# Kernel optimization log

Measured on AMD Instinct MI355X. Metric: run time of the kernel, lower is better.

The kernel has to match this reference:

```python
import jax, jax.numpy as jnp
import numpy as np

N, DIM, E = 50000, 128, 600000


def setup_inputs() -> dict:
    key = jax.random.key(0)
    ks = jax.random.split(key, 10)
    scale = 1.0 / np.sqrt(DIM)
    return {
        "s": jax.random.normal(ks[0], (N, DIM), jnp.float32),
        "v": jax.random.normal(ks[1], (N, 3, DIM), jnp.float32),
        "edge_index": jax.random.randint(ks[2], (2, E), 0, N, jnp.int32),
        # linear_q: Linear(dim, dim); stored as [in, out] so y = x @ W + b
        "Wq": jax.random.normal(ks[3], (DIM, DIM), jnp.float32) * scale,
        "bq": jnp.zeros((DIM,), jnp.float32),
        # linear_kv: Linear(dim, 3*dim)
        "Wkv": jax.random.normal(ks[4], (DIM, 3 * DIM), jnp.float32) * scale,
        "bkv": jnp.zeros((3 * DIM,), jnp.float32),
        # vec_mlp: Linear(dim, dim)
        "Wvec": jax.random.normal(ks[5], (DIM, DIM), jnp.float32) * scale,
        "bvec": jnp.zeros((DIM,), jnp.float32),
    }


def reference(s, v, edge_index, Wq, bq, Wkv, bkv, Wvec, bvec):
    n_nodes = s.shape[0]
    row, col = edge_index[0], edge_index[1]

    q = s @ Wq + bq                                   # [N, dim]
    kv = s @ Wkv + bkv                                # [N, 3*dim]
    k, v_s, v_v = jnp.split(kv, 3, axis=-1)           # each [N, dim]

    # edge attention weight: per-edge dot product of gathered q/k
    w = jnp.sum(q[row] * k[col], axis=-1, keepdims=True)   # [E, 1]

    edge_msg_s = w * v_s[col]                               # [E, dim]
    # [E,1,1] * [E,1,dim] * [E,3,dim] -> [E,3,dim]
    edge_msg_v = w[:, :, None] * v_v[col][:, None, :] * v[col]

    agg_s = jax.ops.segment_sum(edge_msg_s, row, num_segments=n_nodes)  # [N, dim]
    agg_v = jax.ops.segment_sum(edge_msg_v, row, num_segments=n_nodes)  # [N, 3, dim]

    s_out = s + agg_s
    v_out = v + (agg_v @ Wvec + bvec)
    return (s_out, v_out)
```

## Files before the change

### kernel.cpp

```cpp
#include <hip/hip_runtime.h>
#include <hip/hip_bf16.h>

typedef __attribute__((ext_vector_type(8))) __bf16 bf16x8;
typedef __attribute__((ext_vector_type(4))) float f32x4;


__global__ void prep_kernel(const int* __restrict__ row, int* __restrict__ cnt, int e,
                            const float* __restrict__ Wq, const float* __restrict__ Wkv,
                            const float* __restrict__ Wvec, const float* __restrict__ bq,
                            const float* __restrict__ bkv,
                            __bf16* __restrict__ Wt, float* __restrict__ bM,
                            float* __restrict__ m2, float* __restrict__ c0, int nbh) {
  const int bid = blockIdx.x, tid = threadIdx.x;
  if (bid < nbh) {
    int i = bid * 256 + tid;
    if (i < e) atomicAdd(&cnt[row[i]], 1);
  } else if (bid < nbh + 256) {
    int idx = (bid - nbh) * 256 + tid;
    int c = 128 + (idx >> 7), k = idx & 127;
    float w = (c < 512) ? Wkv[k * 384 + (c - 128)] : Wvec[k * 128 + (c - 512)];
    Wt[c * 128 + k] = (__bf16)w;
  } else if (bid < nbh + 256 + 128) {
    __shared__ float wk[128];
    int c = bid - (nbh + 256);
    if (tid < 128) wk[tid] = Wkv[c * 384 + tid];
    __syncthreads();
    if (tid < 128) {
      float acc = 0.f;
      #pragma unroll 8
      for (int j = 0; j < 128; j++) acc += Wq[tid * 128 + j] * wk[j];
      Wt[c * 128 + tid] = (__bf16)acc;
    } else if (tid == 128) {
      float acc = 0.f;
      for (int j = 0; j < 128; j++) acc += bq[j] * wk[j];
      bM[c] = acc;
    }
  } else {
    if (tid < 128) {
      float acc = 0.f;
      for (int j = 0; j < 128; j++) acc += Wq[tid * 128 + j] * bkv[j];
      m2[tid] = acc;
    } else if (tid == 128) {
      float acc = 0.f;
      for (int j = 0; j < 128; j++) acc += bq[j] * bkv[j];
      c0[0] = acc;
    }
  }
}

__global__ __launch_bounds__(1024) void scan1_kernel(const int* __restrict__ cnt, int* __restrict__ off,
                                                     int* __restrict__ bsum, int n) {
  __shared__ int sh[1024];
  int tid = threadIdx.x;
  int i = blockIdx.x * 1024 + tid;
  int v = (i < n) ? cnt[i] : 0;
  sh[tid] = v;
  __syncthreads();
  for (int d = 1; d < 1024; d <<= 1) {
    int t = (tid >= d) ? sh[tid - d] : 0;
    __syncthreads();
    sh[tid] += t;
    __syncthreads();
  }
  if (i < n) off[i] = sh[tid] - v;
  if (tid == 1023) bsum[blockIdx.x] = sh[1023];
}

__global__ __launch_bounds__(1024) void scan3_kernel(const int* __restrict__ bsum, int* __restrict__ off,
                                                     int* __restrict__ cursor, int n, int e) {
  __shared__ int base_sh;
  const int tid = threadIdx.x;
  if (tid < 64) {
    int part = 0;
    for (int b = tid; b < (int)blockIdx.x; b += 64) part += bsum[b];
    #pragma unroll
    for (int m = 32; m >= 1; m >>= 1) part += __shfl_xor(part, m);
    if (tid == 0) base_sh = part;
  }
  __syncthreads();
  const int base = base_sh;
  int i = blockIdx.x * 1024 + tid;
  if (i < n) { int o = off[i] + base; off[i] = o; cursor[i] = o; }
  if (i == 0) off[n] = e;
}


__global__ __launch_bounds__(256) void scatter_gemm1(
    const int* __restrict__ row, const int* __restrict__ col,
    int* __restrict__ cursor, int* __restrict__ scol, int e, int ngemm,
    const float* __restrict__ s, const __bf16* __restrict__ Wtg,
    const float* __restrict__ bM, const float* __restrict__ bkv,
    const float* __restrict__ m2, const float* __restrict__ c0,
    const float* __restrict__ v,
    __bf16* __restrict__ qb, float* __restrict__ beta,
    __bf16* __restrict__ nodebuf, int n)
{
  __shared__ __bf16 sA[64 * 136];
  __shared__ char uB[34816];
  __shared__ float sBeta[64][4];
  __bf16* sB = (__bf16*)uB;
  float*  sO = (float*)uB;

  const int tid = threadIdx.x;
  if ((int)blockIdx.x >= ngemm) {
    int i = ((int)blockIdx.x - ngemm) * 256 + tid;
    if (i < e) { int r = row[i]; int pos = atomicAdd(&cursor[r], 1); scol[pos] = col[i]; }
    return;
  }

  const int nb1 = (n + 63) >> 6;
  const int y = ((int)blockIdx.x < nb1) ? 0 : 1;
  const int n0 = (y == 0 ? (int)blockIdx.x : (int)blockIdx.x - nb1) * 64;
  const int drow = tid >> 2, dseg = tid & 3;
  const int dgn = n0 + drow;

  {
    float4 f[8];
    if (dgn < n) {
      #pragma unroll
      for (int i = 0; i < 8; i++)
        f[i] = *(const float4*)&s[(size_t)dgn * 128 + dseg * 32 + i * 4];
    } else {
      #pragma unroll
      for (int i = 0; i < 8; i++) f[i] = make_float4(0.f, 0.f, 0.f, 0.f);
    }
    #pragma unroll
    for (int i = 0; i < 4; i++) {
      bf16x8 pk;
      pk[0] = (__bf16)f[2*i].x;   pk[1] = (__bf16)f[2*i].y;
      pk[2] = (__bf16)f[2*i].z;   pk[3] = (__bf16)f[2*i].w;
      pk[4] = (__bf16)f[2*i+1].x; pk[5] = (__bf16)f[2*i+1].y;
      pk[6] = (__bf16)f[2*i+1].z; pk[7] = (__bf16)f[2*i+1].w;
      *(bf16x8*)&sA[drow * 136 + dseg * 32 + i * 8] = pk;
    }
  }
  {
    int r2 = tid >> 1, half = tid & 1;
    int brow = (y == 0) ? r2 : 384 + r2;
    const __bf16* src = &Wtg[(size_t)brow * 128 + half * 64];
    #pragma unroll
    for (int i = 0; i < 8; i++)
      *(bf16x8*)&sB[r2 * 136 + half * 64 + i * 8] = *(const bf16x8*)&src[i * 8];
  }
  __syncthreads();

  const int wave = tid >> 6, lane = tid & 63;
  const int lr = lane & 15, lg = lane >> 4;

  bf16x8 a[4];
  #pragma unroll
  for (int ks = 0; ks < 4; ks++)
    a[ks] = *(const bf16x8*)&sA[(wave * 16 + lr) * 136 + ks * 32 + lg * 8];

  f32x4 acc[8];
  #pragma unroll
  for (int cf = 0; cf < 8; cf++) {
    f32x4 c = {0.f, 0.f, 0.f, 0.f};
    #pragma unroll
    for (int ks = 0; ks < 4; ks++) {
      bf16x8 b = *(const bf16x8*)&sB[(cf * 16 + lr) * 136 + ks * 32 + lg * 8];
      c = __builtin_amdgcn_mfma_f32_16x16x32_bf16(a[ks], b, c, 0, 0, 0);
    }
    acc[cf] = c;
  }
  __syncthreads();

  #pragma unroll
  for (int cf = 0; cf < 8; cf++) {
    int cl = cf * 16 + lr;
    #pragma unroll
    for (int r = 0; r < 4; r++)
      sO[(wave * 16 + lg * 4 + r) * 132 + cl] = acc[cf][r];
  }
  __syncthreads();

  if (y == 0) {
    float part = 0.f;
    #pragma unroll 8
    for (int j = 0; j < 32; j++)
      part += (float)sA[drow * 136 + dseg * 32 + j] * m2[dseg * 32 + j];
    sBeta[drow][dseg] = part;
    __syncthreads();
    if (dgn < n) {
      if (dseg == 0)
        beta[dgn] = sBeta[drow][0] + sBeta[drow][1] + sBeta[drow][2] + sBeta[drow][3] + c0[0];
      #pragma unroll
      for (int i = 0; i < 4; i++) {
        int cc = dseg * 32 + i * 8;
        bf16x8 pk;
        #pragma unroll
        for (int j = 0; j < 8; j++)
          pk[j] = (__bf16)(sO[drow * 132 + cc + j] + bM[cc + j]);
        *(bf16x8*)&qb[(size_t)dgn * 128 + cc] = pk;
      }
    }
  } else if (dgn < n) {
    #pragma unroll
    for (int i = 0; i < 4; i++) {
      int cc = dseg * 32 + i * 8;
      *(bf16x8*)&nodebuf[(size_t)dgn * 512 + cc] = *(const bf16x8*)&sA[drow * 136 + cc];
    }
    float vv[32];
    #pragma unroll
    for (int j = 0; j < 32; j++)
      vv[j] = sO[drow * 132 + dseg * 32 + j] + bkv[256 + dseg * 32 + j];
    #pragma unroll
    for (int j3 = 0; j3 < 3; j3++) {
      #pragma unroll
      for (int i = 0; i < 4; i++) {
        int cc = dseg * 32 + i * 8;
        float4 va = *(const float4*)&v[((size_t)dgn * 3 + j3) * 128 + cc];
        float4 vb = *(const float4*)&v[((size_t)dgn * 3 + j3) * 128 + cc + 4];
        bf16x8 pk;
        pk[0] = (__bf16)(vv[i*8+0] * va.x); pk[1] = (__bf16)(vv[i*8+1] * va.y);
        pk[2] = (__bf16)(vv[i*8+2] * va.z); pk[3] = (__bf16)(vv[i*8+3] * va.w);
        pk[4] = (__bf16)(vv[i*8+4] * vb.x); pk[5] = (__bf16)(vv[i*8+5] * vb.y);
        pk[6] = (__bf16)(vv[i*8+6] * vb.z); pk[7] = (__bf16)(vv[i*8+7] * vb.w);
        *(bf16x8*)&nodebuf[(size_t)dgn * 512 + 128 + j3 * 128 + cc] = pk;
      }
    }
  }
}


__device__ inline float2 bf2f(unsigned u) {
  float2 r;
  r.x = __uint_as_float((u & 0xffffu) << 16);
  r.y = __uint_as_float(u & 0xffff0000u);
  return r;
}

__device__ __forceinline__ float dpp_add(float x, const int ctrl) {
  int t;
  switch (ctrl) {
    case 0:  t = __builtin_amdgcn_update_dpp(0, __float_as_int(x), 0xB1, 0xF, 0xF, true); break;
    case 1:  t = __builtin_amdgcn_update_dpp(0, __float_as_int(x), 0x4E, 0xF, 0xF, true); break;
    case 2:  t = __builtin_amdgcn_update_dpp(0, __float_as_int(x), 0x141, 0xF, 0xF, true); break;
    default: t = __builtin_amdgcn_update_dpp(0, __float_as_int(x), 0x140, 0xF, 0xF, true); break;
  }
  return x + __int_as_float(t);
}

__device__ __forceinline__ float row16_sum(float x) {
  x = dpp_add(x, 0); x = dpp_add(x, 1); x = dpp_add(x, 2); x = dpp_add(x, 3);
  return x;
}

#define ACCP(arr, vec) do { float2 _t;                                                \
  _t = bf2f(vec.x); arr[0].x = fmaf(d, _t.x, arr[0].x); arr[0].y = fmaf(d, _t.y, arr[0].y); \
  _t = bf2f(vec.y); arr[1].x = fmaf(d, _t.x, arr[1].x); arr[1].y = fmaf(d, _t.y, arr[1].y); \
  _t = bf2f(vec.z); arr[2].x = fmaf(d, _t.x, arr[2].x); arr[2].y = fmaf(d, _t.y, arr[2].y); \
  _t = bf2f(vec.w); arr[3].x = fmaf(d, _t.x, arr[3].x); arr[3].y = fmaf(d, _t.y, arr[3].y); \
} while (0)

__global__ __launch_bounds__(256) void agg_kernel(
    const int* __restrict__ off, const int* __restrict__ scol,
    const __bf16* __restrict__ qb, const float* __restrict__ beta,
    const char* __restrict__ nodebuf,
    __bf16* __restrict__ gb, float* __restrict__ W1,
    __bf16* __restrict__ aggv16, int n)
{
  const int wid = threadIdx.x >> 6;
  const int lane = threadIdx.x & 63;
  const int nid = blockIdx.x * 4 + wid;
  if (nid >= n) return;
  const int slot = lane >> 4;
  const int fl = lane & 15;

  float qf[8];
  {
    uint4 qu = *(const uint4*)&qb[(size_t)nid * 128 + fl * 8];
    float2 t;
    t = bf2f(qu.x); qf[0] = t.x; qf[1] = t.y;
    t = bf2f(qu.y); qf[2] = t.x; qf[3] = t.y;
    t = bf2f(qu.z); qf[4] = t.x; qf[5] = t.y;
    t = bf2f(qu.w); qf[6] = t.x; qf[7] = t.y;
  }
  const float betar = beta[nid];

  float2 g[4], a0[4], a1[4], a2[4];
  float ws = 0.f;
  #pragma unroll
  for (int i = 0; i < 4; i++) {
    g[i] = make_float2(0.f, 0.f); a0[i] = make_float2(0.f, 0.f);
    a1[i] = make_float2(0.f, 0.f); a2[i] = make_float2(0.f, 0.f);
  }

  const int beg = off[nid];
  const int deg = off[nid + 1] - beg;

  for (int chunk = 0; chunk < deg; chunk += 64) {
    const int cc = (deg - chunk < 64) ? (deg - chunk) : 64;
    int myc = (lane < cc) ? scol[beg + chunk + lane] : 0;

    int c0i = __shfl(myc, (slot < cc) ? slot : 0);
    const char* gp = nodebuf + (size_t)c0i * 1024 + fl * 16;
    uint4 sc = *(const uint4*)(gp);
    uint4 p0 = *(const uint4*)(gp + 256);
    uint4 p1 = *(const uint4*)(gp + 512);
    uint4 p2 = *(const uint4*)(gp + 768);

    for (int j = 0; j < cc; j += 4) {
      const bool more = (j + 4 < cc);
      uint4 nsc, np0, np1, np2;
      if (more) {
        int ni = j + 4 + slot;
        int cn = __shfl(myc, (ni < cc) ? ni : 0);
        const char* gn = nodebuf + (size_t)cn * 1024 + fl * 16;
        nsc = *(const uint4*)(gn);
        np0 = *(const uint4*)(gn + 256);
        np1 = *(const uint4*)(gn + 512);
        np2 = *(const uint4*)(gn + 768);
      }

      float2 t0 = bf2f(sc.x), t1 = bf2f(sc.y), t2 = bf2f(sc.z), t3 = bf2f(sc.w);
      float d = 0.f;
      d = fmaf(qf[0], t0.x, d); d = fmaf(qf[1], t0.y, d);
      d = fmaf(qf[2], t1.x, d); d = fmaf(qf[3], t1.y, d);
      d = fmaf(qf[4], t2.x, d); d = fmaf(qf[5], t2.y, d);
      d = fmaf(qf[6], t3.x, d); d = fmaf(qf[7], t3.y, d);
      d = row16_sum(d) + betar;
      if (j + slot >= cc) d = 0.f;

      g[0].x = fmaf(d, t0.x, g[0].x); g[0].y = fmaf(d, t0.y, g[0].y);
      g[1].x = fmaf(d, t1.x, g[1].x); g[1].y = fmaf(d, t1.y, g[1].y);
      g[2].x = fmaf(d, t2.x, g[2].x); g[2].y = fmaf(d, t2.y, g[2].y);
      g[3].x = fmaf(d, t3.x, g[3].x); g[3].y = fmaf(d, t3.y, g[3].y);
      ws += d;
      ACCP(a0, p0); ACCP(a1, p1); ACCP(a2, p2);

      if (more) { sc = nsc; p0 = np0; p1 = np1; p2 = np2; }
    }
  }

  ws += __shfl_xor(ws, 16); ws += __shfl_xor(ws, 32);
  #pragma unroll
  for (int i = 0; i < 4; i++) {
    g[i].x  += __shfl_xor(g[i].x, 16);  g[i].x  += __shfl_xor(g[i].x, 32);
    g[i].y  += __shfl_xor(g[i].y, 16);  g[i].y  += __shfl_xor(g[i].y, 32);
    a0[i].x += __shfl_xor(a0[i].x, 16); a0[i].x += __shfl_xor(a0[i].x, 32);
    a0[i].y += __shfl_xor(a0[i].y, 16); a0[i].y += __shfl_xor(a0[i].y, 32);
    a1[i].x += __shfl_xor(a1[i].x, 16); a1[i].x += __shfl_xor(a1[i].x, 32);
    a1[i].y += __shfl_xor(a1[i].y, 16); a1[i].y += __shfl_xor(a1[i].y, 32);
    a2[i].x += __shfl_xor(a2[i].x, 16); a2[i].x += __shfl_xor(a2[i].x, 32);
    a2[i].y += __shfl_xor(a2[i].y, 16); a2[i].y += __shfl_xor(a2[i].y, 32);
  }

  if (slot == 0) {
    bf16x8 pk;
    pk[0] = (__bf16)g[0].x; pk[1] = (__bf16)g[0].y; pk[2] = (__bf16)g[1].x; pk[3] = (__bf16)g[1].y;
    pk[4] = (__bf16)g[2].x; pk[5] = (__bf16)g[2].y; pk[6] = (__bf16)g[3].x; pk[7] = (__bf16)g[3].y;
    *(bf16x8*)&gb[(size_t)nid * 128 + fl * 8] = pk;
    if (fl == 0) W1[nid] = ws;

    pk[0] = (__bf16)a0[0].x; pk[1] = (__bf16)a0[0].y; pk[2] = (__bf16)a0[1].x; pk[3] = (__bf16)a0[1].y;
    pk[4] = (__bf16)a0[2].x; pk[5] = (__bf16)a0[2].y; pk[6] = (__bf16)a0[3].x; pk[7] = (__bf16)a0[3].y;
    *(bf16x8*)&aggv16[((size_t)nid * 3 + 0) * 128 + fl * 8] = pk;
    pk[0] = (__bf16)a1[0].x; pk[1] = (__bf16)a1[0].y; pk[2] = (__bf16)a1[1].x; pk[3] = (__bf16)a1[1].y;
    pk[4] = (__bf16)a1[2].x; pk[5] = (__bf16)a1[2].y; pk[6] = (__bf16)a1[3].x; pk[7] = (__bf16)a1[3].y;
    *(bf16x8*)&aggv16[((size_t)nid * 3 + 1) * 128 + fl * 8] = pk;
    pk[0] = (__bf16)a2[0].x; pk[1] = (__bf16)a2[0].y; pk[2] = (__bf16)a2[1].x; pk[3] = (__bf16)a2[1].y;
    pk[4] = (__bf16)a2[2].x; pk[5] = (__bf16)a2[2].y; pk[6] = (__bf16)a2[3].x; pk[7] = (__bf16)a2[3].y;
    *(bf16x8*)&aggv16[((size_t)nid * 3 + 2) * 128 + fl * 8] = pk;
  }
}


__global__ __launch_bounds__(256) void gemm23_mfma(
    const __bf16* __restrict__ Wtg, const float* __restrict__ bkv, const float* __restrict__ bvec,
    const float* __restrict__ s, const float* __restrict__ v,
    const __bf16* __restrict__ gb, const float* __restrict__ W1,
    const __bf16* __restrict__ aggv16,
    float* __restrict__ s_out, float* __restrict__ vout, int n, int nb1)
{
  __shared__ __bf16 sA[64 * 136];
  __shared__ char uB[34816];
  __bf16* sB = (__bf16*)uB;
  float*  sO = (float*)uB;

  const int tid = threadIdx.x;
  const bool smode = (int)blockIdx.x < nb1;
  const int r0 = smode ? blockIdx.x * 64 : (blockIdx.x - nb1) * 64;
  const int rows = smode ? n : 3 * n;
  const int drow = tid >> 2, dseg = tid & 3;
  const int dgr = r0 + drow;

  {
    const __bf16* Asrc = smode ? gb : aggv16;
    #pragma unroll
    for (int i = 0; i < 4; i++) {
      bf16x8 pk = {0,0,0,0,0,0,0,0};
      if (dgr < rows) pk = *(const bf16x8*)&Asrc[(size_t)dgr * 128 + dseg * 32 + i * 8];
      *(bf16x8*)&sA[drow * 136 + dseg * 32 + i * 8] = pk;
    }
  }
  {
    int r2 = tid >> 1, half = tid & 1;
    int brow = (smode ? 256 : 512) + r2;
    const __bf16* src = &Wtg[(size_t)brow * 128 + half * 64];
    #pragma unroll
    for (int i = 0; i < 8; i++)
      *(bf16x8*)&sB[r2 * 136 + half * 64 + i * 8] = *(const bf16x8*)&src[i * 8];
  }
  __syncthreads();

  const int wave = tid >> 6, lane = tid & 63;
  const int lr = lane & 15, lg = lane >> 4;

  bf16x8 a[4];
  #pragma unroll
  for (int ks = 0; ks < 4; ks++)
    a[ks] = *(const bf16x8*)&sA[(wave * 16 + lr) * 136 + ks * 32 + lg * 8];

  f32x4 acc[8];
  #pragma unroll
  for (int cf = 0; cf < 8; cf++) {
    f32x4 c = {0.f, 0.f, 0.f, 0.f};
    #pragma unroll
    for (int ks = 0; ks < 4; ks++) {
      bf16x8 b = *(const bf16x8*)&sB[(cf * 16 + lr) * 136 + ks * 32 + lg * 8];
      c = __builtin_amdgcn_mfma_f32_16x16x32_bf16(a[ks], b, c, 0, 0, 0);
    }
    acc[cf] = c;
  }
  __syncthreads();

  #pragma unroll
  for (int cf = 0; cf < 8; cf++) {
    int cl = cf * 16 + lr;
    #pragma unroll
    for (int r = 0; r < 4; r++)
      sO[(wave * 16 + lg * 4 + r) * 132 + cl] = acc[cf][r];
  }
  __syncthreads();

  if (dgr < rows) {
    if (smode) {
      const float w1 = W1[dgr];
      #pragma unroll
      for (int i = 0; i < 8; i++) {
        int cc = dseg * 32 + i * 4;
        float4 sa = *(const float4*)&s[(size_t)dgr * 128 + cc];
        float4 o;
        o.x = sO[drow * 132 + cc + 0] + sa.x + w1 * bkv[128 + cc + 0];
        o.y = sO[drow * 132 + cc + 1] + sa.y + w1 * bkv[128 + cc + 1];
        o.z = sO[drow * 132 + cc + 2] + sa.z + w1 * bkv[128 + cc + 2];
        o.w = sO[drow * 132 + cc + 3] + sa.w + w1 * bkv[128 + cc + 3];
        *(float4*)&s_out[(size_t)dgr * 128 + cc] = o;
      }
    } else {
      #pragma unroll
      for (int i = 0; i < 8; i++) {
        int cc = dseg * 32 + i * 4;
        float4 va = *(const float4*)&v[(size_t)dgr * 128 + cc];
        float4 o;
        o.x = sO[drow * 132 + cc + 0] + va.x + bvec[cc + 0];
        o.y = sO[drow * 132 + cc + 1] + va.y + bvec[cc + 1];
        o.z = sO[drow * 132 + cc + 2] + va.z + bvec[cc + 2];
        o.w = sO[drow * 132 + cc + 3] + va.w + bvec[cc + 3];
        *(float4*)&vout[(size_t)dgr * 128 + cc] = o;
      }
    }
  }
}


extern "C" void kernel_launch(void* const* d_in, const int* in_sizes, int n_in,
                              void* d_out, int out_size, void* d_ws, size_t ws_size,
                              hipStream_t stream)
{
  const float* s    = (const float*)d_in[0];
  const float* v    = (const float*)d_in[1];
  const int*   ei   = (const int*)d_in[2];
  const float* Wq   = (const float*)d_in[3];
  const float* bq   = (const float*)d_in[4];
  const float* Wkv  = (const float*)d_in[5];
  const float* bkv  = (const float*)d_in[6];
  const float* Wvec = (const float*)d_in[7];
  const float* bvec = (const float*)d_in[8];

  const int N = in_sizes[0] / 128;
  const int E = in_sizes[2] / 2;
  const int* row = ei;
  const int* col = ei + E;

  char* ws = (char*)d_ws;
  size_t o = 0;
  auto alloc = [&](size_t bytes) -> char* {
    char* p = ws + o;
    o = (o + bytes + 255) & ~(size_t)255;
    return p;
  };
  int* off    = (int*)alloc((size_t)(N + 1) * 4);
  int* cursor = (int*)alloc((size_t)N * 4);
  int* bsum   = (int*)alloc(4096);
  int* scol   = (int*)alloc((size_t)E * 4);
  __bf16* qb      = (__bf16*)alloc((size_t)N * 128 * 2);
  float*  beta    = (float*)alloc((size_t)N * 4);
  float*  W1      = (float*)alloc((size_t)N * 4);
  __bf16* nodebuf = (__bf16*)alloc((size_t)N * 512 * 2);
  __bf16* Wt      = (__bf16*)alloc((size_t)640 * 128 * 2);
  __bf16* aggv16  = (__bf16*)alloc((size_t)N * 384 * 2);
  __bf16* gb      = (__bf16*)alloc((size_t)N * 128 * 2);
  float*  bM      = (float*)alloc(512);
  float*  m2      = (float*)alloc(512);
  float*  c0      = (float*)alloc(256);

  float* s_out = (float*)d_out;
  float* vout  = (float*)d_out + (size_t)N * 128;

  hipMemsetAsync(cursor, 0, (size_t)N * 4, stream);
  int nbh = (E + 255) / 256;
  prep_kernel<<<nbh + 256 + 128 + 1, 256, 0, stream>>>(row, cursor, E, Wq, Wkv, Wvec, bq, bkv,
                                                       Wt, bM, m2, c0, nbh);
  int nb = (N + 1023) / 1024;
  scan1_kernel<<<nb, 1024, 0, stream>>>(cursor, off, bsum, N);
  scan3_kernel<<<nb, 1024, 0, stream>>>(bsum, off, cursor, N, E);

  int nb1 = (N + 63) / 64;
  int ngemm = 2 * nb1;
  int nbs = (E + 255) / 256;
  scatter_gemm1<<<ngemm + nbs, 256, 0, stream>>>(row, col, cursor, scol, E, ngemm,
                                                 s, Wt, bM, bkv, m2, c0, v,
                                                 qb, beta, nodebuf, N);

  agg_kernel<<<(N + 3) / 4, 256, 0, stream>>>(off, scol, qb, beta, (const char*)nodebuf,
                                              gb, W1, aggv16, N);

  int nb2 = (3 * N + 63) / 64;
  gemm23_mfma<<<nb1 + nb2, 256, 0, stream>>>(Wt, bkv, bvec, s, v, gb, W1, aggv16,
                                             s_out, vout, N, nb1);
}
```

Measured before the change: 284.7 us.

## Split scatter from gemm1 and load MFMA A fragments directly from global

The edge scatter is moved out of the fused scatter+GEMM launch into its own kernel, and gemm1 now uses a 2D grid. In both GEMM kernels the A operand is loaded straight from global memory into per-lane MFMA fragments instead of being staged through a shared-memory tile. This cuts LDS usage and one barrier, and the beta dot product is computed from registers with cross-lane shuffles. The cost is an extra kernel launch, the loss of overlap between scatter and GEMM, and less coalesced global reads for A.

```diff
diff --git a/kernel.cpp b/kernel.cpp
--- a/kernel.cpp
+++ b/kernel.cpp
@@ -84,10 +84,14 @@
   if (i == 0) off[n] = e;
 }
 
-
-__global__ __launch_bounds__(256) void scatter_gemm1(
-    const int* __restrict__ row, const int* __restrict__ col,
-    int* __restrict__ cursor, int* __restrict__ scol, int e, int ngemm,
+__global__ void scatter_kernel(const int* __restrict__ row, const int* __restrict__ col,
+                               int* __restrict__ cursor, int* __restrict__ scol, int e) {
+  int i = blockIdx.x * 256 + threadIdx.x;
+  if (i < e) { int r = row[i]; int pos = atomicAdd(&cursor[r], 1); scol[pos] = col[i]; }
+}
+
+
+__global__ __launch_bounds__(256) void gemm1_mfma(
     const float* __restrict__ s, const __bf16* __restrict__ Wtg,
     const float* __restrict__ bM, const float* __restrict__ bkv,
     const float* __restrict__ m2, const float* __restrict__ c0,
@@ -95,45 +99,17 @@
     __bf16* __restrict__ qb, float* __restrict__ beta,
     __bf16* __restrict__ nodebuf, int n)
 {
-  __shared__ __bf16 sA[64 * 136];
   __shared__ char uB[34816];
-  __shared__ float sBeta[64][4];
   __bf16* sB = (__bf16*)uB;
   float*  sO = (float*)uB;
 
   const int tid = threadIdx.x;
-  if ((int)blockIdx.x >= ngemm) {
-    int i = ((int)blockIdx.x - ngemm) * 256 + tid;
-    if (i < e) { int r = row[i]; int pos = atomicAdd(&cursor[r], 1); scol[pos] = col[i]; }
-    return;
-  }
-
-  const int nb1 = (n + 63) >> 6;
-  const int y = ((int)blockIdx.x < nb1) ? 0 : 1;
-  const int n0 = (y == 0 ? (int)blockIdx.x : (int)blockIdx.x - nb1) * 64;
-  const int drow = tid >> 2, dseg = tid & 3;
-  const int dgn = n0 + drow;
-
-  {
-    float4 f[8];
-    if (dgn < n) {
-      #pragma unroll
-      for (int i = 0; i < 8; i++)
-        f[i] = *(const float4*)&s[(size_t)dgn * 128 + dseg * 32 + i * 4];
-    } else {
-      #pragma unroll
-      for (int i = 0; i < 8; i++) f[i] = make_float4(0.f, 0.f, 0.f, 0.f);
-    }
-    #pragma unroll
-    for (int i = 0; i < 4; i++) {
-      bf16x8 pk;
-      pk[0] = (__bf16)f[2*i].x;   pk[1] = (__bf16)f[2*i].y;
-      pk[2] = (__bf16)f[2*i].z;   pk[3] = (__bf16)f[2*i].w;
-      pk[4] = (__bf16)f[2*i+1].x; pk[5] = (__bf16)f[2*i+1].y;
-      pk[6] = (__bf16)f[2*i+1].z; pk[7] = (__bf16)f[2*i+1].w;
-      *(bf16x8*)&sA[drow * 136 + dseg * 32 + i * 8] = pk;
-    }
-  }
+  const int y = blockIdx.y;
+  const int n0 = blockIdx.x * 64;
+  const int wave = tid >> 6, lane = tid & 63;
+  const int lr = lane & 15, lg = lane >> 4;
+  const int arow = n0 + wave * 16 + lr;
+
   {
     int r2 = tid >> 1, half = tid & 1;
     int brow = (y == 0) ? r2 : 384 + r2;
@@ -142,15 +118,23 @@
     for (int i = 0; i < 8; i++)
       *(bf16x8*)&sB[r2 * 136 + half * 64 + i * 8] = *(const bf16x8*)&src[i * 8];
   }
-  __syncthreads();
-
-  const int wave = tid >> 6, lane = tid & 63;
-  const int lr = lane & 15, lg = lane >> 4;
 
   bf16x8 a[4];
-  #pragma unroll
-  for (int ks = 0; ks < 4; ks++)
-    a[ks] = *(const bf16x8*)&sA[(wave * 16 + lr) * 136 + ks * 32 + lg * 8];
+  if (arow < n) {
+    #pragma unroll
+    for (int ks = 0; ks < 4; ks++) {
+      float4 f0 = *(const float4*)&s[(size_t)arow * 128 + ks * 32 + lg * 8];
+      float4 f1 = *(const float4*)&s[(size_t)arow * 128 + ks * 32 + lg * 8 + 4];
+      bf16x8 pk;
+      pk[0] = (__bf16)f0.x; pk[1] = (__bf16)f0.y; pk[2] = (__bf16)f0.z; pk[3] = (__bf16)f0.w;
+      pk[4] = (__bf16)f1.x; pk[5] = (__bf16)f1.y; pk[6] = (__bf16)f1.z; pk[7] = (__bf16)f1.w;
+      a[ks] = pk;
+    }
+  } else {
+    #pragma unroll
+    for (int ks = 0; ks < 4; ks++) a[ks] = bf16x8{0,0,0,0,0,0,0,0};
+  }
+  __syncthreads();
 
   f32x4 acc[8];
   #pragma unroll
@@ -174,16 +158,21 @@
   }
   __syncthreads();
 
+  const int drow = tid >> 2, dseg = tid & 3;
+  const int dgn = n0 + drow;
+
   if (y == 0) {
     float part = 0.f;
-    #pragma unroll 8
-    for (int j = 0; j < 32; j++)
-      part += (float)sA[drow * 136 + dseg * 32 + j] * m2[dseg * 32 + j];
-    sBeta[drow][dseg] = part;
-    __syncthreads();
+    #pragma unroll
+    for (int ks = 0; ks < 4; ks++)
+      #pragma unroll
+      for (int j = 0; j < 8; j++)
+        part += (float)a[ks][j] * m2[ks * 32 + lg * 8 + j];
+    part += __shfl_xor(part, 16);
+    part += __shfl_xor(part, 32);
+    if (lane < 16 && arow < n) beta[arow] = part + c0[0];
+
     if (dgn < n) {
-      if (dseg == 0)
-        beta[dgn] = sBeta[drow][0] + sBeta[drow][1] + sBeta[drow][2] + sBeta[drow][3] + c0[0];
       #pragma unroll
       for (int i = 0; i < 4; i++) {
         int cc = dseg * 32 + i * 8;
@@ -194,29 +183,31 @@
         *(bf16x8*)&qb[(size_t)dgn * 128 + cc] = pk;
       }
     }
-  } else if (dgn < n) {
-    #pragma unroll
-    for (int i = 0; i < 4; i++) {
-      int cc = dseg * 32 + i * 8;
-      *(bf16x8*)&nodebuf[(size_t)dgn * 512 + cc] = *(const bf16x8*)&sA[drow * 136 + cc];
-    }
-    float vv[32];
-    #pragma unroll
-    for (int j = 0; j < 32; j++)
-      vv[j] = sO[drow * 132 + dseg * 32 + j] + bkv[256 + dseg * 32 + j];
-    #pragma unroll
-    for (int j3 = 0; j3 < 3; j3++) {
-      #pragma unroll
-      for (int i = 0; i < 4; i++) {
-        int cc = dseg * 32 + i * 8;
-        float4 va = *(const float4*)&v[((size_t)dgn * 3 + j3) * 128 + cc];
-        float4 vb = *(const float4*)&v[((size_t)dgn * 3 + j3) * 128 + cc + 4];
-        bf16x8 pk;
-        pk[0] = (__bf16)(vv[i*8+0] * va.x); pk[1] = (__bf16)(vv[i*8+1] * va.y);
-        pk[2] = (__bf16)(vv[i*8+2] * va.z); pk[3] = (__bf16)(vv[i*8+3] * va.w);
-        pk[4] = (__bf16)(vv[i*8+4] * vb.x); pk[5] = (__bf16)(vv[i*8+5] * vb.y);
-        pk[6] = (__bf16)(vv[i*8+6] * vb.z); pk[7] = (__bf16)(vv[i*8+7] * vb.w);
-        *(bf16x8*)&nodebuf[(size_t)dgn * 512 + 128 + j3 * 128 + cc] = pk;
+  } else {
+    if (arow < n) {
+      #pragma unroll
+      for (int ks = 0; ks < 4; ks++)
+        *(bf16x8*)&nodebuf[(size_t)arow * 512 + ks * 32 + lg * 8] = a[ks];
+    }
+    if (dgn < n) {
+      float vv[32];
+      #pragma unroll
+      for (int j = 0; j < 32; j++)
+        vv[j] = sO[drow * 132 + dseg * 32 + j] + bkv[256 + dseg * 32 + j];
+      #pragma unroll
+      for (int j3 = 0; j3 < 3; j3++) {
+        #pragma unroll
+        for (int i = 0; i < 4; i++) {
+          int cc = dseg * 32 + i * 8;
+          float4 va = *(const float4*)&v[((size_t)dgn * 3 + j3) * 128 + cc];
+          float4 vb = *(const float4*)&v[((size_t)dgn * 3 + j3) * 128 + cc + 4];
+          bf16x8 pk;
+          pk[0] = (__bf16)(vv[i*8+0] * va.x); pk[1] = (__bf16)(vv[i*8+1] * va.y);
+          pk[2] = (__bf16)(vv[i*8+2] * va.z); pk[3] = (__bf16)(vv[i*8+3] * va.w);
+          pk[4] = (__bf16)(vv[i*8+4] * vb.x); pk[5] = (__bf16)(vv[i*8+5] * vb.y);
+          pk[6] = (__bf16)(vv[i*8+6] * vb.z); pk[7] = (__bf16)(vv[i*8+7] * vb.w);
+          *(bf16x8*)&nodebuf[(size_t)dgn * 512 + 128 + j3 * 128 + cc] = pk;
+        }
       }
     }
   }
@@ -373,7 +364,6 @@
     const __bf16* __restrict__ aggv16,
     float* __restrict__ s_out, float* __restrict__ vout, int n, int nb1)
 {
-  __shared__ __bf16 sA[64 * 136];
   __shared__ char uB[34816];
   __bf16* sB = (__bf16*)uB;
   float*  sO = (float*)uB;
@@ -382,18 +372,10 @@
   const bool smode = (int)blockIdx.x < nb1;
   const int r0 = smode ? blockIdx.x * 64 : (blockIdx.x - nb1) * 64;
   const int rows = smode ? n : 3 * n;
-  const int drow = tid >> 2, dseg = tid & 3;
-  const int dgr = r0 + drow;
-
-  {
-    const __bf16* Asrc = smode ? gb : aggv16;
-    #pragma unroll
-    for (int i = 0; i < 4; i++) {
-      bf16x8 pk = {0,0,0,0,0,0,0,0};
-      if (dgr < rows) pk = *(const bf16x8*)&Asrc[(size_t)dgr * 128 + dseg * 32 + i * 8];
-      *(bf16x8*)&sA[drow * 136 + dseg * 32 + i * 8] = pk;
-    }
-  }
+  const int wave = tid >> 6, lane = tid & 63;
+  const int lr = lane & 15, lg = lane >> 4;
+  const int arow = r0 + wave * 16 + lr;
+
   {
     int r2 = tid >> 1, half = tid & 1;
     int brow = (smode ? 256 : 512) + r2;
@@ -402,15 +384,18 @@
     for (int i = 0; i < 8; i++)
       *(bf16x8*)&sB[r2 * 136 + half * 64 + i * 8] = *(const bf16x8*)&src[i * 8];
   }
-  __syncthreads();
-
-  const int wave = tid >> 6, lane = tid & 63;
-  const int lr = lane & 15, lg = lane >> 4;
-
+
+  const __bf16* Asrc = smode ? gb : aggv16;
   bf16x8 a[4];
-  #pragma unroll
-  for (int ks = 0; ks < 4; ks++)
-    a[ks] = *(const bf16x8*)&sA[(wave * 16 + lr) * 136 + ks * 32 + lg * 8];
+  if (arow < rows) {
+    #pragma unroll
+    for (int ks = 0; ks < 4; ks++)
+      a[ks] = *(const bf16x8*)&Asrc[(size_t)arow * 128 + ks * 32 + lg * 8];
+  } else {
+    #pragma unroll
+    for (int ks = 0; ks < 4; ks++) a[ks] = bf16x8{0,0,0,0,0,0,0,0};
+  }
+  __syncthreads();
 
   f32x4 acc[8];
   #pragma unroll
@@ -433,6 +418,9 @@
       sO[(wave * 16 + lg * 4 + r) * 132 + cl] = acc[cf][r];
   }
   __syncthreads();
+
+  const int drow = tid >> 2, dseg = tid & 3;
+  const int dgr = r0 + drow;
 
   if (dgr < rows) {
     if (smode) {
@@ -516,13 +504,11 @@
   int nb = (N + 1023) / 1024;
   scan1_kernel<<<nb, 1024, 0, stream>>>(cursor, off, bsum, N);
   scan3_kernel<<<nb, 1024, 0, stream>>>(bsum, off, cursor, N, E);
+  scatter_kernel<<<(E + 255) / 256, 256, 0, stream>>>(row, col, cursor, scol, E);
 
   int nb1 = (N + 63) / 64;
-  int ngemm = 2 * nb1;
-  int nbs = (E + 255) / 256;
-  scatter_gemm1<<<ngemm + nbs, 256, 0, stream>>>(row, col, cursor, scol, E, ngemm,
-                                                 s, Wt, bM, bkv, m2, c0, v,
-                                                 qb, beta, nodebuf, N);
+  dim3 g1(nb1, 2);
+  gemm1_mfma<<<g1, 256, 0, stream>>>(s, Wt, bM, bkv, m2, c0, v, qb, beta, nodebuf, N);
 
   agg_kernel<<<(N + 3) / 4, 256, 0, stream>>>(off, scol, qb, beta, (const char*)nodebuf,
                                               gb, W1, aggv16, N);
```

New measurement: 289.6 us. About the same (+1.7%).
